# Kernel optimization log

Measured on AMD Instinct MI355X. Metric: run time of the kernel, lower is better.

Reference implementation:

```python
import jax, jax.numpy as jnp
import numpy as np

N = 100000
E = 1600000
EPS = 1e-16
NEG_SLOPE = 0.2


def setup_inputs() -> dict:
    key = jax.random.key(0)
    ks = jax.random.split(key, 10)
    F_in, C = 512, 40
    H1, D1 = 8, 8
    return {
        "x": jax.random.normal(ks[0], (N, F_in), jnp.float32),
        "edge_index": jax.random.randint(ks[1], (2, E), 0, N, jnp.int64),
        "W1": jax.random.normal(ks[2], (F_in, H1 * D1), jnp.float32) * 0.05,
        "att_src1": jax.random.normal(ks[3], (H1, D1), jnp.float32) * 0.1,
        "att_dst1": jax.random.normal(ks[4], (H1, D1), jnp.float32) * 0.1,
        "b1": jnp.zeros((H1 * D1,), jnp.float32),
        "W2": jax.random.normal(ks[5], (H1 * D1, C), jnp.float32) * 0.05,
        "att_src2": jax.random.normal(ks[6], (1, C), jnp.float32) * 0.1,
        "att_dst2": jax.random.normal(ks[7], (1, C), jnp.float32) * 0.1,
        "b2": jnp.zeros((C,), jnp.float32),
    }


def gat_conv(x, W, att_src, att_dst, bias, src, dst, heads, out_dim, concat):
    # Linear transform per head: [N, H, D]
    h = (x @ W).reshape(N, heads, out_dim)
    # Per-node attention logits: [N, H]
    a_src = jnp.einsum("nhd,hd->nh", h, att_src)
    a_dst = jnp.einsum("nhd,hd->nh", h, att_dst)
    # Per-edge logits (edge j->i: src=j, softmax grouped by dst=i)
    e = a_src[src] + a_dst[dst]                      # [E', H]
    e = jax.nn.leaky_relu(e, NEG_SLOPE)
    # Segment softmax over destination nodes (numerically stable)
    m = jax.ops.segment_max(e, dst, num_segments=N)  # [N, H]
    e = jnp.exp(e - m[dst])
    s = jax.ops.segment_sum(e, dst, num_segments=N)  # [N, H]
    alpha = e / (s[dst] + EPS)                       # [E', H]
    # Weighted message aggregation (scatter-add)
    msg = h[src] * alpha[:, :, None]                 # [E', H, D]
    out = jax.ops.segment_sum(msg, dst, num_segments=N)  # [N, H, D]
    out = out.reshape(N, heads * out_dim) if concat else out.mean(axis=1)
    return out + bias


def reference(x, edge_index, W1, att_src1, att_dst1, b1, W2, att_src2, att_dst2, b2):
    # PyG GATConv default: add self-loops
    loops = jnp.arange(N, dtype=edge_index.dtype)
    src = jnp.concatenate([edge_index[0], loops])
    dst = jnp.concatenate([edge_index[1], loops])
    h = gat_conv(x, W1, att_src1, att_dst1, b1, src, dst, heads=8, out_dim=8, concat=True)
    h = jax.nn.elu(h)
    out = gat_conv(h, W2, att_src2, att_dst2, b2, src, dst, heads=1, out_dim=40, concat=False)
    return jax.nn.log_softmax(out, axis=1)
```

## Files before the change

### kernel.cpp

```cpp
#include <hip/hip_runtime.h>
#include <cstdint>

#define N_NODES 100000
#define N_EDGES 1600000
#define ETOT    1700000
#define FIN     512
#define HD1     64
#define NB      80
#define C2      40
#define NEG_SLOPE 0.2f
#define SCAN_NB ((N_NODES + 1023) / 1024)

typedef __attribute__((ext_vector_type(8))) short bf16x8;
typedef __attribute__((ext_vector_type(4))) float f32x4;

__device__ __forceinline__ float lrelu(float v) { return v > 0.f ? v : NEG_SLOPE * v; }

__device__ __forceinline__ unsigned short f2bf(float f) {
    uint32_t u = __float_as_uint(f);
    u += 0x7FFF + ((u >> 16) & 1);
    return (unsigned short)(u >> 16);
}
__device__ __forceinline__ float bf2f(unsigned short u) {
    return __uint_as_float(((uint32_t)u) << 16);
}

__global__ void k_prep(const float* __restrict__ W1, const float* __restrict__ a_s,
                       const float* __restrict__ a_d,
                       const float* __restrict__ W2, const float* __restrict__ att_s2,
                       const float* __restrict__ att_d2,
                       unsigned short* __restrict__ W1t, unsigned short* __restrict__ W2t) {
    if (blockIdx.x < 160) {
        int t = blockIdx.x * 256 + threadIdx.x;
        int n = t >> 9, k = t & 511;
        float v;
        if (n < 64) {
            v = W1[k * HD1 + n];
        } else if (n < 72) {
            int h = n - 64; v = 0.f;
#pragma unroll
            for (int d = 0; d < 8; d++) v += W1[k * HD1 + h * 8 + d] * a_s[h * 8 + d];
        } else {
            int h = n - 72; v = 0.f;
#pragma unroll
            for (int d = 0; d < 8; d++) v += W1[k * HD1 + h * 8 + d] * a_d[h * 8 + d];
        }
        W1t[n * FIN + k] = f2bf(v);
    } else {
        int t = (blockIdx.x - 160) * 256 + threadIdx.x;
        if (t >= 48 * 64) return;
        int n = t >> 6, k = t & 63;
        float v = 0.f;
        if (n < C2) {
            v = W2[k * C2 + n];
        } else if (n == C2) {
            for (int c = 0; c < C2; c++) v += W2[k * C2 + c] * att_s2[c];
        } else if (n == C2 + 1) {
            for (int c = 0; c < C2; c++) v += W2[k * C2 + c] * att_d2[c];
        }
        W2t[n * 64 + k] = f2bf(v);
    }
}

__global__ __launch_bounds__(256) void k_gemm1(const float* __restrict__ x,
                                               const unsigned short* __restrict__ W1t,
                                               unsigned short* __restrict__ h1b,
                                               float* __restrict__ as1,
                                               float* __restrict__ ad1) {
    __shared__ unsigned short As[128 * 72];
    const int t    = threadIdx.x;
    const int lane = t & 63, wv = t >> 6;
    const int quad = lane >> 4, l16 = lane & 15;
    const int row0 = blockIdx.x * 128;

    f32x4 acc[2][5];
#pragma unroll
    for (int mi = 0; mi < 2; mi++)
#pragma unroll
        for (int ni = 0; ni < 5; ni++) acc[mi][ni] = (f32x4){0.f, 0.f, 0.f, 0.f};

    float4 rx[8];
#pragma unroll
    for (int i = 0; i < 8; i++) {
        int ff = t + i * 256;
        int r = ff >> 4, c4 = ff & 15;
        int row = row0 + r;
        rx[i] = (row < N_NODES) ? *(const float4*)&x[(size_t)row * FIN + c4 * 4]
                                : make_float4(0.f, 0.f, 0.f, 0.f);
    }

    for (int c = 0; c < 8; c++) {
#pragma unroll
        for (int i = 0; i < 8; i++) {
            int ff = t + i * 256;
            int r = ff >> 4, c4 = ff & 15;
            ushort4 s4;
            s4.x = f2bf(rx[i].x); s4.y = f2bf(rx[i].y);
            s4.z = f2bf(rx[i].z); s4.w = f2bf(rx[i].w);
            *(ushort4*)&As[r * 72 + c4 * 4] = s4;
        }
        __syncthreads();
        if (c < 7) {
            int kb = (c + 1) * 64;
#pragma unroll
            for (int i = 0; i < 8; i++) {
                int ff = t + i * 256;
                int r = ff >> 4, c4 = ff & 15;
                int row = row0 + r;
                rx[i] = (row < N_NODES) ? *(const float4*)&x[(size_t)row * FIN + kb + c4 * 4]
                                        : make_float4(0.f, 0.f, 0.f, 0.f);
            }
        }
        int kb = c * 64;
#pragma unroll
        for (int ks = 0; ks < 2; ks++) {
            bf16x8 af[2], bfv[5];
#pragma unroll
            for (int mi = 0; mi < 2; mi++) {
                int lr = wv * 32 + mi * 16 + l16;
                af[mi] = *(const bf16x8*)&As[lr * 72 + ks * 32 + quad * 8];
            }
#pragma unroll
            for (int ni = 0; ni < 5; ni++) {
                int n = ni * 16 + l16;
                bfv[ni] = *(const bf16x8*)&W1t[n * FIN + kb + ks * 32 + quad * 8];
            }
#pragma unroll
            for (int mi = 0; mi < 2; mi++)
#pragma unroll
                for (int ni = 0; ni < 5; ni++)
                    acc[mi][ni] = __builtin_amdgcn_mfma_f32_16x16x32_bf16(
                        af[mi], bfv[ni], acc[mi][ni], 0, 0, 0);
        }
        __syncthreads();
    }
#pragma unroll
    for (int mi = 0; mi < 2; mi++)
#pragma unroll
        for (int ni = 0; ni < 5; ni++)
#pragma unroll
            for (int r = 0; r < 4; r++) {
                int row = row0 + wv * 32 + mi * 16 + quad * 4 + r;
                if (row >= N_NODES) continue;
                int col = ni * 16 + l16;
                float v = acc[mi][ni][r];
                if (col < 64)       h1b[(size_t)row * 64 + col] = f2bf(v);
                else if (col < 72)  as1[row * 8 + (col - 64)] = v;
                else                ad1[row * 8 + (col - 72)] = v;
            }
}

__global__ void k_deg(const int* __restrict__ ei, int* __restrict__ deg) {
    int e = blockIdx.x * 256 + threadIdx.x;
    if (e >= ETOT) return;
    int dst = (e < N_EDGES) ? ei[N_EDGES + e] : e - N_EDGES;
    atomicAdd(&deg[dst], 1);
}

__global__ __launch_bounds__(1024) void k_bsum(const int* __restrict__ deg,
                                               int* __restrict__ bsum) {
    __shared__ int wsm[16];
    int t = threadIdx.x;
    int i = blockIdx.x * 1024 + t;
    int v = (i < N_NODES) ? deg[i] : 0;
#pragma unroll
    for (int o = 32; o >= 1; o >>= 1) v += __shfl_xor(v, o, 64);
    if ((t & 63) == 0) wsm[t >> 6] = v;
    __syncthreads();
    if (t < 16) {
        int s = wsm[t];
#pragma unroll
        for (int o = 8; o >= 1; o >>= 1) s += __shfl_xor(s, o, 16);
        if (t == 0) bsum[blockIdx.x] = s;
    }
}

__global__ __launch_bounds__(128) void k_bscan(const int* __restrict__ bsum,
                                               int* __restrict__ boff) {
    __shared__ int sh[128];
    int t = threadIdx.x;
    int v = (t < SCAN_NB) ? bsum[t] : 0;
    sh[t] = v;
    __syncthreads();
    for (int off = 1; off < 128; off <<= 1) {
        int u = (t >= off) ? sh[t - off] : 0;
        __syncthreads();
        sh[t] += u;
        __syncthreads();
    }
    boff[t] = sh[t] - v;
}

__global__ __launch_bounds__(1024) void k_scan3(const int* __restrict__ deg,
                                                const int* __restrict__ boff,
                                                int* __restrict__ row_ptr) {
    __shared__ int sh[1024];
    int t = threadIdx.x;
    int i = blockIdx.x * 1024 + t;
    int v = (i < N_NODES) ? deg[i] : 0;
    sh[t] = v;
    __syncthreads();
    for (int off = 1; off < 1024; off <<= 1) {
        int u = (t >= off) ? sh[t - off] : 0;
        __syncthreads();
        sh[t] += u;
        __syncthreads();
    }
    int base = boff[blockIdx.x];
    if (i < N_NODES) row_ptr[i] = base + sh[t] - v;
    if (i == N_NODES - 1) row_ptr[N_NODES] = base + sh[t];
}

__global__ void k_scatter(const int* __restrict__ ei, const int* __restrict__ row_ptr,
                          int* __restrict__ cnt, int* __restrict__ csr_src) {
    int e = blockIdx.x * 256 + threadIdx.x;
    if (e >= ETOT) return;
    int src, dst;
    if (e < N_EDGES) { src = ei[e]; dst = ei[N_EDGES + e]; }
    else             { src = dst = e - N_EDGES; }
    int pos = row_ptr[dst] + atomicAdd(&cnt[dst], 1);
    csr_src[pos] = src;
}

__global__ __launch_bounds__(256) void k_agg1(
    const unsigned short* __restrict__ h1b,
    const float* __restrict__ as1, const float* __restrict__ ad1,
    const int* __restrict__ row_ptr, const int* __restrict__ csr_src,
    const float* __restrict__ b1, unsigned short* __restrict__ hb) {
    int t = threadIdx.x, wv = t >> 6, lane = t & 63;
    int dst = blockIdx.x * 4 + wv;
    if (dst >= N_NODES) return;
    int h = lane >> 3;
    int s0 = row_ptr[dst], s1e = row_ptr[dst + 1];
    float adh = ad1[dst * 8 + h];
    float acc = 0.f, den = 0.f;
    for (int base = s0; base < s1e; base += 64) {
        int idx = base + lane;
        int sl = (idx < s1e) ? csr_src[idx] : 0;
        int cnt = min(64, s1e - base);
        int j = 0;
        for (; j + 4 <= cnt; j += 4) {
#pragma unroll
            for (int jj = 0; jj < 4; jj++) {
                int s = __shfl(sl, j + jj);
                float w = __expf(lrelu(as1[s * 8 + h] + adh));
                den += w;
                acc += w * bf2f(h1b[(size_t)s * 64 + lane]);
            }
        }
        for (; j < cnt; j++) {
            int s = __shfl(sl, j);
            float w = __expf(lrelu(as1[s * 8 + h] + adh));
            den += w;
            acc += w * bf2f(h1b[(size_t)s * 64 + lane]);
        }
    }
    float hv = acc / (den + 1e-16f) + b1[lane];
    hv = hv > 0.f ? hv : expm1f(hv);
    hb[(size_t)dst * 64 + lane] = f2bf(hv);
}

__global__ __launch_bounds__(256) void k_gemm2(const unsigned short* __restrict__ hb,
                                               const unsigned short* __restrict__ W2t,
                                               unsigned short* __restrict__ h2b,
                                               float* __restrict__ as2,
                                               float* __restrict__ ad2) {
    const int t = threadIdx.x;
    const int lane = t & 63, wv = t >> 6;
    const int quad = lane >> 4, l16 = lane & 15;
    const int row0 = blockIdx.x * 128;

    f32x4 acc[2][3];
#pragma unroll
    for (int mi = 0; mi < 2; mi++)
#pragma unroll
        for (int ni = 0; ni < 3; ni++) acc[mi][ni] = (f32x4){0.f, 0.f, 0.f, 0.f};

    bf16x8 bfrag[2][3];
#pragma unroll
    for (int ks = 0; ks < 2; ks++)
#pragma unroll
        for (int ni = 0; ni < 3; ni++)
            bfrag[ks][ni] = *(const bf16x8*)&W2t[(ni * 16 + l16) * 64 + ks * 32 + quad * 8];

#pragma unroll
    for (int mi = 0; mi < 2; mi++) {
        int row = row0 + wv * 32 + mi * 16 + l16;
        int rowc = row < N_NODES ? row : N_NODES - 1;
#pragma unroll
        for (int ks = 0; ks < 2; ks++) {
            bf16x8 af = *(const bf16x8*)&hb[(size_t)rowc * 64 + ks * 32 + quad * 8];
#pragma unroll
            for (int ni = 0; ni < 3; ni++)
                acc[mi][ni] = __builtin_amdgcn_mfma_f32_16x16x32_bf16(
                    af, bfrag[ks][ni], acc[mi][ni], 0, 0, 0);
        }
    }
#pragma unroll
    for (int mi = 0; mi < 2; mi++)
#pragma unroll
        for (int ni = 0; ni < 3; ni++)
#pragma unroll
            for (int r = 0; r < 4; r++) {
                int row = row0 + wv * 32 + mi * 16 + quad * 4 + r;
                if (row >= N_NODES) continue;
                int col = ni * 16 + l16;
                float v = acc[mi][ni][r];
                if (col < C2)            h2b[(size_t)row * C2 + col] = f2bf(v);
                else if (col == C2)      as2[row] = v;
                else if (col == C2 + 1)  ad2[row] = v;
            }
}

__global__ __launch_bounds__(256) void k_agg2(
    const unsigned short* __restrict__ h2b,
    const float* __restrict__ as2, const float* __restrict__ ad2,
    const int* __restrict__ row_ptr, const int* __restrict__ csr_src,
    const float* __restrict__ b2, float* __restrict__ out) {
    int t = threadIdx.x, wv = t >> 6, lane = t & 63;
    int dst = blockIdx.x * 4 + wv;
    if (dst >= N_NODES) return;
    int s0 = row_ptr[dst], s1e = row_ptr[dst + 1];
    float ad = ad2[dst];
    bool act = lane < C2;
    int cl = act ? lane : 0;
    float acc = 0.f, den = 0.f;
    for (int base = s0; base < s1e; base += 64) {
        int idx = base + lane;
        bool vld = idx < s1e;
        int sl = vld ? csr_src[idx] : 0;
        float wl = vld ? __expf(lrelu(as2[sl] + ad)) : 0.f;
        float d = wl;
#pragma unroll
        for (int o = 32; o >= 1; o >>= 1) d += __shfl_xor(d, o, 64);
        den += d;
        int cnt  = min(64, s1e - base);
        int cnt4 = (cnt + 3) & ~3;
        for (int j = 0; j < cnt4; j += 4) {
#pragma unroll
            for (int jj = 0; jj < 4; jj++) {
                int s   = __shfl(sl, j + jj);
                float w = __shfl(wl, j + jj);
                float hvv = bf2f(h2b[(size_t)s * C2 + cl]);
                if (act) acc += w * hvv;
            }
        }
    }
    float v = act ? acc / (den + 1e-16f) + b2[cl] : -1e30f;
    float m = v;
#pragma unroll
    for (int o = 32; o >= 1; o >>= 1) m = fmaxf(m, __shfl_xor(m, o, 64));
    float ex = act ? __expf(v - m) : 0.f;
    float ssum = ex;
#pragma unroll
    for (int o = 32; o >= 1; o >>= 1) ssum += __shfl_xor(ssum, o, 64);
    if (act) out[(size_t)dst * C2 + lane] = v - m - logf(ssum);
}

extern "C" void kernel_launch(void* const* d_in, const int* in_sizes, int n_in,
                              void* d_out, int out_size, void* d_ws, size_t ws_size,
                              hipStream_t stream) {
    const float* x     = (const float*)d_in[0];
    const int*   ei    = (const int*)d_in[1];
    const float* W1    = (const float*)d_in[2];
    const float* at_s1 = (const float*)d_in[3];
    const float* at_d1 = (const float*)d_in[4];
    const float* b1    = (const float*)d_in[5];
    const float* W2    = (const float*)d_in[6];
    const float* at_s2 = (const float*)d_in[7];
    const float* at_d2 = (const float*)d_in[8];
    const float* b2    = (const float*)d_in[9];
    float* out = (float*)d_out;
    float* ws  = (float*)d_ws;

    unsigned short* h1b = (unsigned short*)ws;
    float* as1 = ws + 3200000;
    float* ad1 = ws + 4000000;
    unsigned short* hb  = (unsigned short*)(ws + 4800000);
    unsigned short* h2b = (unsigned short*)(ws + 8000000);
    float* as2 = ws + 10000000;
    float* ad2 = ws + 10100000;
    unsigned short* W1t = (unsigned short*)(ws + 10200000);
    unsigned short* W2t = (unsigned short*)(ws + 10250000);
    int* row_ptr = (int*)(ws + 10300000);
    int* deg     = (int*)(ws + 10410000);
    int* cnt     = (int*)(ws + 10520000);
    int* csr_src = (int*)(ws + 10630000);
    int* bsum    = (int*)(ws + 12340000);
    int* boff    = (int*)(ws + 12350000);

    hipMemsetAsync(deg, 0, (size_t)N_NODES * sizeof(int), stream);
    hipMemsetAsync(cnt, 0, (size_t)N_NODES * sizeof(int), stream);

    k_prep<<<172, 256, 0, stream>>>(W1, at_s1, at_d1, W2, at_s2, at_d2, W1t, W2t);
    k_deg<<<(ETOT + 255) / 256, 256, 0, stream>>>(ei, deg);
    k_bsum<<<SCAN_NB, 1024, 0, stream>>>(deg, bsum);
    k_bscan<<<1, 128, 0, stream>>>(bsum, boff);
    k_scan3<<<SCAN_NB, 1024, 0, stream>>>(deg, boff, row_ptr);
    k_scatter<<<(ETOT + 255) / 256, 256, 0, stream>>>(ei, row_ptr, cnt, csr_src);
    k_gemm1<<<(N_NODES + 127) / 128, 256, 0, stream>>>(x, W1t, h1b, as1, ad1);
    k_agg1<<<(N_NODES + 3) / 4, 256, 0, stream>>>(h1b, as1, ad1, row_ptr, csr_src, b1, hb);
    k_gemm2<<<(N_NODES + 127) / 128, 256, 0, stream>>>(hb, W2t, h2b, as2, ad2);
    k_agg2<<<(N_NODES + 3) / 4, 256, 0, stream>>>(h2b, as2, ad2, row_ptr, csr_src, b2, out);
}
```

Baseline: 616.8 us.

## Fuse all GAT stages into one cooperative persistent kernel with grid syncs

Replaces the chain of separate kernel launches and memsets with a single cooperative kernel that runs nine phases separated by grid-wide syncs. A fallback runs the same phases as separate launches. Along the way it records each edge's slot from the degree atomic so the CSR scatter needs no second atomic counter. It also runs the CSR scatter on a quarter of the blocks while the rest do the first GEMM, and restructures the GEMM tiles for 512-thread blocks. This is meant to remove launch overhead and idle gaps between stages. The cost is grid-sync latency, a grid sized for occupancy, and fewer blocks on the bandwidth-heavy aggregation phases.

New measurement: 1.402 ms. 127% more time.

```diff
diff --git a/kernel.cpp b/kernel.cpp
--- a/kernel.cpp
+++ b/kernel.cpp
@@ -1,18 +1,30 @@
 #include <hip/hip_runtime.h>
+#include <hip/hip_cooperative_groups.h>
 #include <cstdint>
+
+namespace cg = cooperative_groups;
 
 #define N_NODES 100000
 #define N_EDGES 1600000
 #define ETOT    1700000
 #define FIN     512
 #define HD1     64
-#define NB      80
 #define C2      40
 #define NEG_SLOPE 0.2f
-#define SCAN_NB ((N_NODES + 1023) / 1024)
+
+#define BLOCK_T  512
+#define NCH      196
+#define GTILES   782
 
 typedef __attribute__((ext_vector_type(8))) short bf16x8;
 typedef __attribute__((ext_vector_type(4))) float f32x4;
+
+struct GArgs {
+    const float* x; const int* ei;
+    const float* W1; const float* a_s1; const float* a_d1; const float* b1;
+    const float* W2; const float* a_s2; const float* a_d2; const float* b2;
+    float* out; float* ws;
+};
 
 __device__ __forceinline__ float lrelu(float v) { return v > 0.f ? v : NEG_SLOPE * v; }
 
@@ -25,256 +37,253 @@
     return __uint_as_float(((uint32_t)u) << 16);
 }
 
-__global__ void k_prep(const float* __restrict__ W1, const float* __restrict__ a_s,
-                       const float* __restrict__ a_d,
-                       const float* __restrict__ W2, const float* __restrict__ att_s2,
-                       const float* __restrict__ att_d2,
-                       unsigned short* __restrict__ W1t, unsigned short* __restrict__ W2t) {
-    if (blockIdx.x < 160) {
-        int t = blockIdx.x * 256 + threadIdx.x;
-        int n = t >> 9, k = t & 511;
-        float v;
-        if (n < 64) {
-            v = W1[k * HD1 + n];
-        } else if (n < 72) {
-            int h = n - 64; v = 0.f;
-#pragma unroll
-            for (int d = 0; d < 8; d++) v += W1[k * HD1 + h * 8 + d] * a_s[h * 8 + d];
+#define WS_PTRS(ws_)                                              \
+    unsigned short* h1b = (unsigned short*)(ws_);                 \
+    float* as1 = (ws_) + 3200000;                                 \
+    float* ad1 = (ws_) + 4000000;                                 \
+    unsigned short* hb  = (unsigned short*)((ws_) + 4800000);     \
+    unsigned short* h2b = (unsigned short*)((ws_) + 8000000);     \
+    float* as2 = (ws_) + 10000000;                                \
+    float* ad2 = (ws_) + 10100000;                                \
+    unsigned short* W1t = (unsigned short*)((ws_) + 10200000);    \
+    unsigned short* W2t = (unsigned short*)((ws_) + 10250000);    \
+    int* row_ptr = (int*)((ws_) + 10300000);                      \
+    int* deg     = (int*)((ws_) + 10410000);                      \
+    int* ord     = (int*)((ws_) + 10520000);                      \
+    int* csr_src = (int*)((ws_) + 12250000);                      \
+    int* bsum    = (int*)((ws_) + 13960000);                      \
+    int* boff    = (int*)((ws_) + 13970000);                      \
+    (void)h1b; (void)as1; (void)ad1; (void)hb; (void)h2b;         \
+    (void)as2; (void)ad2; (void)W1t; (void)W2t; (void)row_ptr;    \
+    (void)deg; (void)ord; (void)csr_src; (void)bsum; (void)boff;
+
+__device__ void phase0(const GArgs& g) {
+    WS_PTRS(g.ws);
+    const int NTH = gridDim.x * BLOCK_T;
+    const int tg  = blockIdx.x * BLOCK_T + threadIdx.x;
+    for (int i = tg; i < N_NODES; i += NTH) deg[i] = 0;
+    for (int i = tg; i < 80 * 512 + 48 * 64; i += NTH) {
+        if (i < 80 * 512) {
+            int n = i >> 9, k = i & 511;
+            float v;
+            if (n < 64) {
+                v = g.W1[k * HD1 + n];
+            } else if (n < 72) {
+                int h = n - 64; v = 0.f;
+#pragma unroll
+                for (int d = 0; d < 8; d++) v += g.W1[k * HD1 + h * 8 + d] * g.a_s1[h * 8 + d];
+            } else {
+                int h = n - 72; v = 0.f;
+#pragma unroll
+                for (int d = 0; d < 8; d++) v += g.W1[k * HD1 + h * 8 + d] * g.a_d1[h * 8 + d];
+            }
+            W1t[n * FIN + k] = f2bf(v);
         } else {
-            int h = n - 72; v = 0.f;
-#pragma unroll
-            for (int d = 0; d < 8; d++) v += W1[k * HD1 + h * 8 + d] * a_d[h * 8 + d];
-        }
-        W1t[n * FIN + k] = f2bf(v);
-    } else {
-        int t = (blockIdx.x - 160) * 256 + threadIdx.x;
-        if (t >= 48 * 64) return;
-        int n = t >> 6, k = t & 63;
-        float v = 0.f;
-        if (n < C2) {
-            v = W2[k * C2 + n];
-        } else if (n == C2) {
-            for (int c = 0; c < C2; c++) v += W2[k * C2 + c] * att_s2[c];
-        } else if (n == C2 + 1) {
-            for (int c = 0; c < C2; c++) v += W2[k * C2 + c] * att_d2[c];
-        }
-        W2t[n * 64 + k] = f2bf(v);
-    }
-}
-
-__global__ __launch_bounds__(256) void k_gemm1(const float* __restrict__ x,
-                                               const unsigned short* __restrict__ W1t,
-                                               unsigned short* __restrict__ h1b,
-                                               float* __restrict__ as1,
-                                               float* __restrict__ ad1) {
-    __shared__ unsigned short As[128 * 72];
-    const int t    = threadIdx.x;
-    const int lane = t & 63, wv = t >> 6;
+            int j = i - 80 * 512;
+            int n = j >> 6, k = j & 63;
+            float v = 0.f;
+            if (n < C2) {
+                v = g.W2[k * C2 + n];
+            } else if (n == C2) {
+                for (int c = 0; c < C2; c++) v += g.W2[k * C2 + c] * g.a_s2[c];
+            } else if (n == C2 + 1) {
+                for (int c = 0; c < C2; c++) v += g.W2[k * C2 + c] * g.a_d2[c];
+            }
+            W2t[n * 64 + k] = f2bf(v);
+        }
+    }
+}
+
+__device__ void phase1(const GArgs& g) {
+    WS_PTRS(g.ws);
+    const int NTH = gridDim.x * BLOCK_T;
+    const int tg  = blockIdx.x * BLOCK_T + threadIdx.x;
+    for (int e = tg; e < ETOT; e += NTH) {
+        int dst = (e < N_EDGES) ? g.ei[N_EDGES + e] : e - N_EDGES;
+        ord[e] = atomicAdd(&deg[dst], 1);
+    }
+}
+
+__device__ void phase2(const GArgs& g) {
+    WS_PTRS(g.ws);
+    __shared__ int sc[512];
+    const int t = threadIdx.x;
+    for (int ch = blockIdx.x; ch < NCH; ch += gridDim.x) {
+        int base = ch << 9;
+        int i = base + t;
+        int v = (i < N_NODES) ? deg[i] : 0;
+        sc[t] = v;
+        __syncthreads();
+        for (int off = 1; off < 512; off <<= 1) {
+            int u = (t >= off) ? sc[t - off] : 0;
+            __syncthreads();
+            sc[t] += u;
+            __syncthreads();
+        }
+        if (i < N_NODES) row_ptr[i] = sc[t] - v;
+        if (t == 511) bsum[ch] = sc[511];
+        __syncthreads();
+    }
+}
+
+__device__ void phase3(const GArgs& g) {
+    WS_PTRS(g.ws);
+    if (blockIdx.x != 0) return;
+    __shared__ int sc[512];
+    const int t = threadIdx.x;
+    int v = (t < NCH) ? bsum[t] : 0;
+    sc[t] = v;
+    __syncthreads();
+    for (int off = 1; off < 512; off <<= 1) {
+        int u = (t >= off) ? sc[t - off] : 0;
+        __syncthreads();
+        sc[t] += u;
+        __syncthreads();
+    }
+    if (t < NCH) boff[t] = sc[t] - v;
+}
+
+__device__ void phase4(const GArgs& g) {
+    WS_PTRS(g.ws);
+    const int NTH = gridDim.x * BLOCK_T;
+    const int tg  = blockIdx.x * BLOCK_T + threadIdx.x;
+    for (int i = tg; i < N_NODES; i += NTH) row_ptr[i] += boff[i >> 9];
+    if (tg == 0) row_ptr[N_NODES] = ETOT;
+}
+
+__device__ __forceinline__ void gemm1_tile(const GArgs& g, unsigned short* As, int row0) {
+    WS_PTRS(g.ws);
+    const int t = threadIdx.x, lane = t & 63, wv = t >> 6;
     const int quad = lane >> 4, l16 = lane & 15;
-    const int row0 = blockIdx.x * 128;
-
-    f32x4 acc[2][5];
-#pragma unroll
-    for (int mi = 0; mi < 2; mi++)
-#pragma unroll
-        for (int ni = 0; ni < 5; ni++) acc[mi][ni] = (f32x4){0.f, 0.f, 0.f, 0.f};
-
-    float4 rx[8];
-#pragma unroll
-    for (int i = 0; i < 8; i++) {
-        int ff = t + i * 256;
-        int r = ff >> 4, c4 = ff & 15;
-        int row = row0 + r;
-        rx[i] = (row < N_NODES) ? *(const float4*)&x[(size_t)row * FIN + c4 * 4]
+
+    f32x4 acc[5];
+#pragma unroll
+    for (int ni = 0; ni < 5; ni++) acc[ni] = (f32x4){0.f, 0.f, 0.f, 0.f};
+
+    float4 rx[4];
+#pragma unroll
+    for (int i = 0; i < 4; i++) {
+        int ff = t + i * 512;
+        int rr = ff >> 4, c4 = ff & 15;
+        int row = row0 + rr;
+        rx[i] = (row < N_NODES) ? *(const float4*)&g.x[(size_t)row * FIN + c4 * 4]
                                 : make_float4(0.f, 0.f, 0.f, 0.f);
     }
-
     for (int c = 0; c < 8; c++) {
 #pragma unroll
-        for (int i = 0; i < 8; i++) {
-            int ff = t + i * 256;
-            int r = ff >> 4, c4 = ff & 15;
+        for (int i = 0; i < 4; i++) {
+            int ff = t + i * 512;
+            int rr = ff >> 4, c4 = ff & 15;
             ushort4 s4;
             s4.x = f2bf(rx[i].x); s4.y = f2bf(rx[i].y);
             s4.z = f2bf(rx[i].z); s4.w = f2bf(rx[i].w);
-            *(ushort4*)&As[r * 72 + c4 * 4] = s4;
+            *(ushort4*)&As[rr * 72 + c4 * 4] = s4;
         }
         __syncthreads();
         if (c < 7) {
             int kb = (c + 1) * 64;
 #pragma unroll
-            for (int i = 0; i < 8; i++) {
-                int ff = t + i * 256;
-                int r = ff >> 4, c4 = ff & 15;
-                int row = row0 + r;
-                rx[i] = (row < N_NODES) ? *(const float4*)&x[(size_t)row * FIN + kb + c4 * 4]
-                                        : make_float4(0.f, 0.f, 0.f, 0.f);
+            for (int i = 0; i < 4; i++) {
+                int ff = t + i * 512;
+                int rr = ff >> 4, c4 = ff & 15;
+                int row = row0 + rr;
+                rx[i] = (row < N_NODES)
+                            ? *(const float4*)&g.x[(size_t)row * FIN + kb + c4 * 4]
+                            : make_float4(0.f, 0.f, 0.f, 0.f);
             }
         }
         int kb = c * 64;
 #pragma unroll
         for (int ks = 0; ks < 2; ks++) {
-            bf16x8 af[2], bfv[5];
-#pragma unroll
-            for (int mi = 0; mi < 2; mi++) {
-                int lr = wv * 32 + mi * 16 + l16;
-                af[mi] = *(const bf16x8*)&As[lr * 72 + ks * 32 + quad * 8];
-            }
+            bf16x8 af, bfv[5];
+            af = *(const bf16x8*)&As[(wv * 16 + l16) * 72 + ks * 32 + quad * 8];
 #pragma unroll
             for (int ni = 0; ni < 5; ni++) {
                 int n = ni * 16 + l16;
                 bfv[ni] = *(const bf16x8*)&W1t[n * FIN + kb + ks * 32 + quad * 8];
             }
 #pragma unroll
-            for (int mi = 0; mi < 2; mi++)
-#pragma unroll
-                for (int ni = 0; ni < 5; ni++)
-                    acc[mi][ni] = __builtin_amdgcn_mfma_f32_16x16x32_bf16(
-                        af[mi], bfv[ni], acc[mi][ni], 0, 0, 0);
-        }
-        __syncthreads();
-    }
-#pragma unroll
-    for (int mi = 0; mi < 2; mi++)
-#pragma unroll
-        for (int ni = 0; ni < 5; ni++)
-#pragma unroll
-            for (int r = 0; r < 4; r++) {
-                int row = row0 + wv * 32 + mi * 16 + quad * 4 + r;
-                if (row >= N_NODES) continue;
-                int col = ni * 16 + l16;
-                float v = acc[mi][ni][r];
-                if (col < 64)       h1b[(size_t)row * 64 + col] = f2bf(v);
-                else if (col < 72)  as1[row * 8 + (col - 64)] = v;
-                else                ad1[row * 8 + (col - 72)] = v;
-            }
-}
-
-__global__ void k_deg(const int* __restrict__ ei, int* __restrict__ deg) {
-    int e = blockIdx.x * 256 + threadIdx.x;
-    if (e >= ETOT) return;
-    int dst = (e < N_EDGES) ? ei[N_EDGES + e] : e - N_EDGES;
-    atomicAdd(&deg[dst], 1);
-}
-
-__global__ __launch_bounds__(1024) void k_bsum(const int* __restrict__ deg,
-                                               int* __restrict__ bsum) {
-    __shared__ int wsm[16];
-    int t = threadIdx.x;
-    int i = blockIdx.x * 1024 + t;
-    int v = (i < N_NODES) ? deg[i] : 0;
-#pragma unroll
-    for (int o = 32; o >= 1; o >>= 1) v += __shfl_xor(v, o, 64);
-    if ((t & 63) == 0) wsm[t >> 6] = v;
-    __syncthreads();
-    if (t < 16) {
-        int s = wsm[t];
-#pragma unroll
-        for (int o = 8; o >= 1; o >>= 1) s += __shfl_xor(s, o, 16);
-        if (t == 0) bsum[blockIdx.x] = s;
-    }
-}
-
-__global__ __launch_bounds__(128) void k_bscan(const int* __restrict__ bsum,
-                                               int* __restrict__ boff) {
-    __shared__ int sh[128];
-    int t = threadIdx.x;
-    int v = (t < SCAN_NB) ? bsum[t] : 0;
-    sh[t] = v;
-    __syncthreads();
-    for (int off = 1; off < 128; off <<= 1) {
-        int u = (t >= off) ? sh[t - off] : 0;
-        __syncthreads();
-        sh[t] += u;
-        __syncthreads();
-    }
-    boff[t] = sh[t] - v;
-}
-
-__global__ __launch_bounds__(1024) void k_scan3(const int* __restrict__ deg,
-                                                const int* __restrict__ boff,
-                                                int* __restrict__ row_ptr) {
-    __shared__ int sh[1024];
-    int t = threadIdx.x;
-    int i = blockIdx.x * 1024 + t;
-    int v = (i < N_NODES) ? deg[i] : 0;
-    sh[t] = v;
-    __syncthreads();
-    for (int off = 1; off < 1024; off <<= 1) {
-        int u = (t >= off) ? sh[t - off] : 0;
-        __syncthreads();
-        sh[t] += u;
-        __syncthreads();
-    }
-    int base = boff[blockIdx.x];
-    if (i < N_NODES) row_ptr[i] = base + sh[t] - v;
-    if (i == N_NODES - 1) row_ptr[N_NODES] = base + sh[t];
-}
-
-__global__ void k_scatter(const int* __restrict__ ei, const int* __restrict__ row_ptr,
-                          int* __restrict__ cnt, int* __restrict__ csr_src) {
-    int e = blockIdx.x * 256 + threadIdx.x;
-    if (e >= ETOT) return;
-    int src, dst;
-    if (e < N_EDGES) { src = ei[e]; dst = ei[N_EDGES + e]; }
-    else             { src = dst = e - N_EDGES; }
-    int pos = row_ptr[dst] + atomicAdd(&cnt[dst], 1);
-    csr_src[pos] = src;
-}
-
-__global__ __launch_bounds__(256) void k_agg1(
-    const unsigned short* __restrict__ h1b,
-    const float* __restrict__ as1, const float* __restrict__ ad1,
-    const int* __restrict__ row_ptr, const int* __restrict__ csr_src,
-    const float* __restrict__ b1, unsigned short* __restrict__ hb) {
-    int t = threadIdx.x, wv = t >> 6, lane = t & 63;
-    int dst = blockIdx.x * 4 + wv;
-    if (dst >= N_NODES) return;
-    int h = lane >> 3;
-    int s0 = row_ptr[dst], s1e = row_ptr[dst + 1];
-    float adh = ad1[dst * 8 + h];
-    float acc = 0.f, den = 0.f;
-    for (int base = s0; base < s1e; base += 64) {
-        int idx = base + lane;
-        int sl = (idx < s1e) ? csr_src[idx] : 0;
-        int cnt = min(64, s1e - base);
-        int j = 0;
-        for (; j + 4 <= cnt; j += 4) {
-#pragma unroll
-            for (int jj = 0; jj < 4; jj++) {
-                int s = __shfl(sl, j + jj);
+            for (int ni = 0; ni < 5; ni++)
+                acc[ni] = __builtin_amdgcn_mfma_f32_16x16x32_bf16(af, bfv[ni], acc[ni], 0, 0, 0);
+        }
+        __syncthreads();
+    }
+#pragma unroll
+    for (int ni = 0; ni < 5; ni++)
+#pragma unroll
+        for (int r = 0; r < 4; r++) {
+            int row = row0 + wv * 16 + quad * 4 + r;
+            if (row >= N_NODES) continue;
+            int col = ni * 16 + l16;
+            float v = acc[ni][r];
+            if (col < 64)       h1b[(size_t)row * 64 + col] = f2bf(v);
+            else if (col < 72)  as1[row * 8 + (col - 64)] = v;
+            else                ad1[row * 8 + (col - 72)] = v;
+        }
+}
+
+__device__ void phase5(const GArgs& g) {
+    WS_PTRS(g.ws);
+    __shared__ unsigned short As[128 * 72];
+    int nb = gridDim.x;
+    int nscat = nb >> 2; if (nscat < 1) nscat = 1;
+    int nbg = nb - nscat;
+    if ((int)blockIdx.x < nbg) {
+        for (int tile = blockIdx.x; tile < GTILES; tile += nbg)
+            gemm1_tile(g, As, tile * 128);
+    } else {
+        const int t = threadIdx.x;
+        for (int e = ((int)blockIdx.x - nbg) * BLOCK_T + t; e < ETOT; e += nscat * BLOCK_T) {
+            int src, dst;
+            if (e < N_EDGES) { src = g.ei[e]; dst = g.ei[N_EDGES + e]; }
+            else             { src = dst = e - N_EDGES; }
+            csr_src[row_ptr[dst] + ord[e]] = src;
+        }
+    }
+}
+
+__device__ void phase6(const GArgs& g) {
+    WS_PTRS(g.ws);
+    const int t = threadIdx.x, lane = t & 63;
+    const int NWV = (gridDim.x * BLOCK_T) >> 6;
+    const int gw  = (blockIdx.x * BLOCK_T + t) >> 6;
+    const int h = lane >> 3;
+    const float blv = g.b1[lane];
+    for (int dst = gw; dst < N_NODES; dst += NWV) {
+        int s0 = row_ptr[dst], s1e = row_ptr[dst + 1];
+        float adh = ad1[dst * 8 + h];
+        float acc = 0.f, den = 0.f;
+        for (int base = s0; base < s1e; base += 64) {
+            int idx = base + lane;
+            int sl = (idx < s1e) ? csr_src[idx] : 0;
+            int cntv = min(64, s1e - base);
+            int j = 0;
+            for (; j + 4 <= cntv; j += 4) {
+#pragma unroll
+                for (int jj = 0; jj < 4; jj++) {
+                    int s = __shfl(sl, j + jj);
+                    float w = __expf(lrelu(as1[s * 8 + h] + adh));
+                    den += w;
+                    acc += w * bf2f(h1b[(size_t)s * 64 + lane]);
+                }
+            }
+            for (; j < cntv; j++) {
+                int s = __shfl(sl, j);
                 float w = __expf(lrelu(as1[s * 8 + h] + adh));
                 den += w;
                 acc += w * bf2f(h1b[(size_t)s * 64 + lane]);
             }
         }
-        for (; j < cnt; j++) {
-            int s = __shfl(sl, j);
-            float w = __expf(lrelu(as1[s * 8 + h] + adh));
-            den += w;
-            acc += w * bf2f(h1b[(size_t)s * 64 + lane]);
-        }
-    }
-    float hv = acc / (den + 1e-16f) + b1[lane];
-    hv = hv > 0.f ? hv : expm1f(hv);
-    hb[(size_t)dst * 64 + lane] = f2bf(hv);
-}
-
-__global__ __launch_bounds__(256) void k_gemm2(const unsigned short* __restrict__ hb,
-                                               const unsigned short* __restrict__ W2t,
-                                               unsigned short* __restrict__ h2b,
-                                               float* __restrict__ as2,
-                                               float* __restrict__ ad2) {
-    const int t = threadIdx.x;
-    const int lane = t & 63, wv = t >> 6;
+        float hv = acc / (den + 1e-16f) + blv;
+        hv = hv > 0.f ? hv : expm1f(hv);
+        hb[(size_t)dst * 64 + lane] = f2bf(hv);
+    }
+}
+
+__device__ void phase7(const GArgs& g) {
+    WS_PTRS(g.ws);
+    const int t = threadIdx.x, lane = t & 63, wv = t >> 6;
     const int quad = lane >> 4, l16 = lane & 15;
-    const int row0 = blockIdx.x * 128;
-
-    f32x4 acc[2][3];
-#pragma unroll
-    for (int mi = 0; mi < 2; mi++)
-#pragma unroll
-        for (int ni = 0; ni < 3; ni++) acc[mi][ni] = (f32x4){0.f, 0.f, 0.f, 0.f};
 
     bf16x8 bfrag[2][3];
 #pragma unroll
@@ -283,123 +292,154 @@
         for (int ni = 0; ni < 3; ni++)
             bfrag[ks][ni] = *(const bf16x8*)&W2t[(ni * 16 + l16) * 64 + ks * 32 + quad * 8];
 
-#pragma unroll
-    for (int mi = 0; mi < 2; mi++) {
-        int row = row0 + wv * 32 + mi * 16 + l16;
+    for (int tile = blockIdx.x; tile < GTILES; tile += gridDim.x) {
+        int row0 = tile * 128;
+        f32x4 acc2[3];
+#pragma unroll
+        for (int ni = 0; ni < 3; ni++) acc2[ni] = (f32x4){0.f, 0.f, 0.f, 0.f};
+
+        int row = row0 + wv * 16 + l16;
         int rowc = row < N_NODES ? row : N_NODES - 1;
 #pragma unroll
         for (int ks = 0; ks < 2; ks++) {
             bf16x8 af = *(const bf16x8*)&hb[(size_t)rowc * 64 + ks * 32 + quad * 8];
 #pragma unroll
             for (int ni = 0; ni < 3; ni++)
-                acc[mi][ni] = __builtin_amdgcn_mfma_f32_16x16x32_bf16(
-                    af, bfrag[ks][ni], acc[mi][ni], 0, 0, 0);
-        }
-    }
-#pragma unroll
-    for (int mi = 0; mi < 2; mi++)
+                acc2[ni] = __builtin_amdgcn_mfma_f32_16x16x32_bf16(af, bfrag[ks][ni], acc2[ni], 0, 0, 0);
+        }
 #pragma unroll
         for (int ni = 0; ni < 3; ni++)
 #pragma unroll
             for (int r = 0; r < 4; r++) {
-                int row = row0 + wv * 32 + mi * 16 + quad * 4 + r;
-                if (row >= N_NODES) continue;
+                int orow = row0 + wv * 16 + quad * 4 + r;
+                if (orow >= N_NODES) continue;
                 int col = ni * 16 + l16;
-                float v = acc[mi][ni][r];
-                if (col < C2)            h2b[(size_t)row * C2 + col] = f2bf(v);
-                else if (col == C2)      as2[row] = v;
-                else if (col == C2 + 1)  ad2[row] = v;
-            }
-}
-
-__global__ __launch_bounds__(256) void k_agg2(
-    const unsigned short* __restrict__ h2b,
-    const float* __restrict__ as2, const float* __restrict__ ad2,
-    const int* __restrict__ row_ptr, const int* __restrict__ csr_src,
-    const float* __restrict__ b2, float* __restrict__ out) {
-    int t = threadIdx.x, wv = t >> 6, lane = t & 63;
-    int dst = blockIdx.x * 4 + wv;
-    if (dst >= N_NODES) return;
-    int s0 = row_ptr[dst], s1e = row_ptr[dst + 1];
-    float ad = ad2[dst];
-    bool act = lane < C2;
-    int cl = act ? lane : 0;
-    float acc = 0.f, den = 0.f;
-    for (int base = s0; base < s1e; base += 64) {
-        int idx = base + lane;
-        bool vld = idx < s1e;
-        int sl = vld ? csr_src[idx] : 0;
-        float wl = vld ? __expf(lrelu(as2[sl] + ad)) : 0.f;
-        float d = wl;
-#pragma unroll
-        for (int o = 32; o >= 1; o >>= 1) d += __shfl_xor(d, o, 64);
-        den += d;
-        int cnt  = min(64, s1e - base);
-        int cnt4 = (cnt + 3) & ~3;
-        for (int j = 0; j < cnt4; j += 4) {
-#pragma unroll
-            for (int jj = 0; jj < 4; jj++) {
-                int s   = __shfl(sl, j + jj);
-                float w = __shfl(wl, j + jj);
-                float hvv = bf2f(h2b[(size_t)s * C2 + cl]);
-                if (act) acc += w * hvv;
-            }
-        }
-    }
-    float v = act ? acc / (den + 1e-16f) + b2[cl] : -1e30f;
-    float m = v;
-#pragma unroll
-    for (int o = 32; o >= 1; o >>= 1) m = fmaxf(m, __shfl_xor(m, o, 64));
-    float ex = act ? __expf(v - m) : 0.f;
-    float ssum = ex;
-#pragma unroll
-    for (int o = 32; o >= 1; o >>= 1) ssum += __shfl_xor(ssum, o, 64);
-    if (act) out[(size_t)dst * C2 + lane] = v - m - logf(ssum);
+                float v = acc2[ni][r];
+                if (col < C2)            h2b[(size_t)orow * C2 + col] = f2bf(v);
+                else if (col == C2)      as2[orow] = v;
+                else if (col == C2 + 1)  ad2[orow] = v;
+            }
+    }
+}
+
+__device__ void phase8(const GArgs& g) {
+    WS_PTRS(g.ws);
+    const int t = threadIdx.x, lane = t & 63;
+    const int NWV = (gridDim.x * BLOCK_T) >> 6;
+    const int gw  = (blockIdx.x * BLOCK_T + t) >> 6;
+    const bool act = lane < C2;
+    const int cl = act ? lane : 0;
+    const float b2v = act ? g.b2[cl] : 0.f;
+    for (int dst = gw; dst < N_NODES; dst += NWV) {
+        int s0 = row_ptr[dst], s1e = row_ptr[dst + 1];
+        float ad = ad2[dst];
+        float acc = 0.f, den = 0.f;
+        for (int base = s0; base < s1e; base += 64) {
+            int idx = base + lane;
+            bool vld = idx < s1e;
+            int sl = vld ? csr_src[idx] : 0;
+            float wl = vld ? __expf(lrelu(as2[sl] + ad)) : 0.f;
+            float d = wl;
+#pragma unroll
+            for (int o = 32; o >= 1; o >>= 1) d += __shfl_xor(d, o, 64);
+            den += d;
+            int cntv = min(64, s1e - base);
+            int cnt4 = (cntv + 3) & ~3;
+            for (int j = 0; j < cnt4; j += 4) {
+#pragma unroll
+                for (int jj = 0; jj < 4; jj++) {
+                    int s   = __shfl(sl, j + jj);
+                    float w = __shfl(wl, j + jj);
+                    float hvv = bf2f(h2b[(size_t)s * C2 + cl]);
+                    if (act) acc += w * hvv;
+                }
+            }
+        }
+        float v = act ? acc / (den + 1e-16f) + b2v : -1e30f;
+        float m = v;
+#pragma unroll
+        for (int o = 32; o >= 1; o >>= 1) m = fmaxf(m, __shfl_xor(m, o, 64));
+        float ex = act ? __expf(v - m) : 0.f;
+        float ssum = ex;
+#pragma unroll
+        for (int o = 32; o >= 1; o >>= 1) ssum += __shfl_xor(ssum, o, 64);
+        if (act) g.out[(size_t)dst * C2 + lane] = v - m - logf(ssum);
+    }
+}
+
+__global__ __launch_bounds__(BLOCK_T, 4) void k_fused(GArgs g) {
+    cg::grid_group grid = cg::this_grid();
+    phase0(g); __threadfence(); grid.sync();
+    phase1(g); __threadfence(); grid.sync();
+    phase2(g); __threadfence(); grid.sync();
+    phase3(g); __threadfence(); grid.sync();
+    phase4(g); __threadfence(); grid.sync();
+    phase5(g); __threadfence(); grid.sync();
+    phase6(g); __threadfence(); grid.sync();
+    phase7(g); __threadfence(); grid.sync();
+    phase8(g);
+}
+
+template <int P>
+__global__ __launch_bounds__(BLOCK_T, 4) void k_phase(GArgs g) {
+    if constexpr (P == 0) phase0(g);
+    else if constexpr (P == 1) phase1(g);
+    else if constexpr (P == 2) phase2(g);
+    else if constexpr (P == 3) phase3(g);
+    else if constexpr (P == 4) phase4(g);
+    else if constexpr (P == 5) phase5(g);
+    else if constexpr (P == 6) phase6(g);
+    else if constexpr (P == 7) phase7(g);
+    else if constexpr (P == 8) phase8(g);
 }
 
 extern "C" void kernel_launch(void* const* d_in, const int* in_sizes, int n_in,
                               void* d_out, int out_size, void* d_ws, size_t ws_size,
                               hipStream_t stream) {
-    const float* x     = (const float*)d_in[0];
-    const int*   ei    = (const int*)d_in[1];
-    const float* W1    = (const float*)d_in[2];
-    const float* at_s1 = (const float*)d_in[3];
-    const float* at_d1 = (const float*)d_in[4];
-    const float* b1    = (const float*)d_in[5];
-    const float* W2    = (const float*)d_in[6];
-    const float* at_s2 = (const float*)d_in[7];
-    const float* at_d2 = (const float*)d_in[8];
-    const float* b2    = (const float*)d_in[9];
-    float* out = (float*)d_out;
-    float* ws  = (float*)d_ws;
-
-    unsigned short* h1b = (unsigned short*)ws;
-    float* as1 = ws + 3200000;
-    float* ad1 = ws + 4000000;
-    unsigned short* hb  = (unsigned short*)(ws + 4800000);
-    unsigned short* h2b = (unsigned short*)(ws + 8000000);
-    float* as2 = ws + 10000000;
-    float* ad2 = ws + 10100000;
-    unsigned short* W1t = (unsigned short*)(ws + 10200000);
-    unsigned short* W2t = (unsigned short*)(ws + 10250000);
-    int* row_ptr = (int*)(ws + 10300000);
-    int* deg     = (int*)(ws + 10410000);
-    int* cnt     = (int*)(ws + 10520000);
-    int* csr_src = (int*)(ws + 10630000);
-    int* bsum    = (int*)(ws + 12340000);
-    int* boff    = (int*)(ws + 12350000);
-
-    hipMemsetAsync(deg, 0, (size_t)N_NODES * sizeof(int), stream);
-    hipMemsetAsync(cnt, 0, (size_t)N_NODES * sizeof(int), stream);
-
-    k_prep<<<172, 256, 0, stream>>>(W1, at_s1, at_d1, W2, at_s2, at_d2, W1t, W2t);
-    k_deg<<<(ETOT + 255) / 256, 256, 0, stream>>>(ei, deg);
-    k_bsum<<<SCAN_NB, 1024, 0, stream>>>(deg, bsum);
-    k_bscan<<<1, 128, 0, stream>>>(bsum, boff);
-    k_scan3<<<SCAN_NB, 1024, 0, stream>>>(deg, boff, row_ptr);
-    k_scatter<<<(ETOT + 255) / 256, 256, 0, stream>>>(ei, row_ptr, cnt, csr_src);
-    k_gemm1<<<(N_NODES + 127) / 128, 256, 0, stream>>>(x, W1t, h1b, as1, ad1);
-    k_agg1<<<(N_NODES + 3) / 4, 256, 0, stream>>>(h1b, as1, ad1, row_ptr, csr_src, b1, hb);
-    k_gemm2<<<(N_NODES + 127) / 128, 256, 0, stream>>>(hb, W2t, h2b, as2, ad2);
-    k_agg2<<<(N_NODES + 3) / 4, 256, 0, stream>>>(h2b, as2, ad2, row_ptr, csr_src, b2, out);
-}
+    GArgs g;
+    g.x    = (const float*)d_in[0];
+    g.ei   = (const int*)d_in[1];
+    g.W1   = (const float*)d_in[2];
+    g.a_s1 = (const float*)d_in[3];
+    g.a_d1 = (const float*)d_in[4];
+    g.b1   = (const float*)d_in[5];
+    g.W2   = (const float*)d_in[6];
+    g.a_s2 = (const float*)d_in[7];
+    g.a_d2 = (const float*)d_in[8];
+    g.b2   = (const float*)d_in[9];
+    g.out  = (float*)d_out;
+    g.ws   = (float*)d_ws;
+
+    static int mode = -1;
+    static int coopGrid = 0;
+    if (mode < 0) {
+        int perCU = 0;
+        hipError_t e1 = hipOccupancyMaxActiveBlocksPerMultiprocessor(&perCU, k_fused, BLOCK_T, 0);
+        int numCU = 0;
+        hipDeviceProp_t prop;
+        int dev = 0;
+        if (hipGetDevice(&dev) == hipSuccess && hipGetDeviceProperties(&prop, dev) == hipSuccess)
+            numCU = prop.multiProcessorCount;
+        if (numCU <= 0) numCU = 256;
+        coopGrid = (e1 == hipSuccess && perCU > 0) ? perCU * numCU : 0;
+        if (coopGrid > 2048) coopGrid = 2048;
+        mode = (coopGrid >= 64) ? 1 : 0;
+    }
+    if (mode == 1) {
+        void* args[] = {(void*)&g};
+        hipError_t e = hipLaunchCooperativeKernel((const void*)k_fused, dim3(coopGrid),
+                                                  dim3(BLOCK_T), args, 0, stream);
+        if (e != hipSuccess) mode = 0;
+    }
+    if (mode == 0) {
+        k_phase<0><<<512,  BLOCK_T, 0, stream>>>(g);
+        k_phase<1><<<512,  BLOCK_T, 0, stream>>>(g);
+        k_phase<2><<<NCH,  BLOCK_T, 0, stream>>>(g);
+        k_phase<3><<<1,    BLOCK_T, 0, stream>>>(g);
+        k_phase<4><<<512,  BLOCK_T, 0, stream>>>(g);
+        k_phase<5><<<784,  BLOCK_T, 0, stream>>>(g);
+        k_phase<6><<<1024, BLOCK_T, 0, stream>>>(g);
+        k_phase<7><<<782,  BLOCK_T, 0, stream>>>(g);
+        k_phase<8><<<1024, BLOCK_T, 0, stream>>>(g);
+    }
+}
```
